# Kernel tuning notes

Hardware: AMD Instinct MI355X
Metric: run time of the kernel (lower is better)

The kernel has to match this reference:

```python
import jax, jax.numpy as jnp
import numpy as np

B, STATE_DIM, MLP_DIM, H, W = 128, 64, 512, 40, 40
LN_EPS = 1e-5


def _sobel_kernel(c):
    # Per-channel depthwise filters in torch order: [c0_sx, c0_sy, c0_id, c1_sx, ...]
    sx = jnp.array([[-1., 0., 1.], [-2., 0., 2.], [-1., 0., 1.]], jnp.float32)
    sy = jnp.array([[-1., -2., -1.], [0., 0., 0.], [1., 2., 1.]], jnp.float32)
    ident = jnp.array([[0., 0., 0.], [0., 1., 0.], [0., 0., 0.]], jnp.float32)
    k = jnp.stack([sx, sy, ident])[:, None]      # [3, 1, 3, 3]
    return jnp.tile(k, (c, 1, 1, 1))             # [3c, 1, 3, 3]


def setup_inputs() -> dict:
    key = jax.random.key(0)
    ks = jax.random.split(key, 6)
    state_in = jax.random.normal(ks[0], (B, STATE_DIM, H, W), jnp.float32)
    w1 = jax.random.normal(ks[1], (MLP_DIM, 3 * STATE_DIM), jnp.float32) * 0.05
    ln_weight = jax.random.uniform(ks[2], (MLP_DIM, H, W), jnp.float32, 0.5, 1.5)
    ln_bias = jax.random.normal(ks[3], (MLP_DIM, H, W), jnp.float32) * 0.01
    w2 = jax.random.normal(ks[4], (STATE_DIM, MLP_DIM), jnp.float32) * 0.05
    mask = jax.random.randint(ks[5], (H, W), 0, 2, jnp.int32)  # bernoulli(0.5) update mask
    return {"state_in": state_in, "w1": w1, "ln_weight": ln_weight,
            "ln_bias": ln_bias, "w2": w2, "mask": mask}


def reference(state_in, w1, ln_weight, ln_bias, w2, mask):
    C = state_in.shape[1]
    # Depthwise 3x3 sobel/identity perception: [B, C, H, W] -> [B, 3C, H, W]
    kern = _sobel_kernel(C)
    x = jax.lax.conv_general_dilated(
        state_in, kern, window_strides=(1, 1), padding='SAME',
        dimension_numbers=('NCHW', 'OIHW', 'NCHW'), feature_group_count=C)
    # 1x1 conv (no bias): [B, 3C, H, W] -> [B, MLP, H, W]
    x = jnp.einsum('bchw,oc->bohw', x, w1)
    # LayerNorm over (MLP, H, W) per sample, with elementwise affine
    mu = jnp.mean(x, axis=(1, 2, 3), keepdims=True)
    var = jnp.var(x, axis=(1, 2, 3), keepdims=True)
    x = (x - mu) * jax.lax.rsqrt(var + LN_EPS) * ln_weight + ln_bias
    x = jax.nn.relu(x)
    # 1x1 conv back to state channels (zero-init in original; random here for testing)
    x = jnp.einsum('bchw,oc->bohw', x, w2)
    # Stochastic per-pixel update mask, broadcast over batch and channels
    x = x * mask.astype(jnp.float32)
    # Alive mask: 3x3 max-pool on alive channel, stride 1, SAME padding
    live = jax.lax.reduce_window(state_in[:, 3], -jnp.inf, jax.lax.max,
                                 (1, 3, 3), (1, 1, 1), 'SAME')
    live = (live > 0.1).astype(jnp.float32)[:, None]  # [B, 1, H, W]
    return state_in + x * live
```

## Files before the change

### kernel.cpp

```cpp
#include <hip/hip_runtime.h>


typedef unsigned short u16;
typedef unsigned int   u32;
typedef __attribute__((ext_vector_type(8))) u16    ushort8;
typedef __attribute__((ext_vector_type(8))) __bf16 bf16x8;
typedef __attribute__((ext_vector_type(4))) float  f32x4;
typedef __attribute__((ext_vector_type(4))) u32    u32x4;

#define NB   128
#define NC   64
#define K1   192
#define NO   512
#define NHW  1600
#define LN_N 819200.0f

__device__ __forceinline__ u16 f2bf(float f) {
    union { float f; u32 u; } v; v.f = f;
    u32 u = v.u;
    u32 r = u + 0x7fffu + ((u >> 16) & 1u);
    return (u16)(r >> 16);
}
__device__ __forceinline__ float bf2f(u16 h) {
    union { u32 u; float f; } v; v.u = ((u32)h) << 16; return v.f;
}
__device__ __forceinline__ f32x4 mfma16(bf16x8 a, bf16x8 b, f32x4 c) {
    return __builtin_amdgcn_mfma_f32_16x16x32_bf16(a, b, c, 0, 0, 0);
}
__device__ __forceinline__ bf16x8 ldfrag(const u16* p) {
    return *(const bf16x8*)p;
}

__device__ __forceinline__ void load_halo(const float* __restrict__ base, int h,
                                          int wq, float reg[3][12]) {
#pragma unroll
    for (int jj = 0; jj < 3; ++jj) {
        int hh = h + jj - 1;
        bool vh = (unsigned)hh < 40u;
        const float* rowp = base + hh * 40;
#pragma unroll
        for (int i = 0; i < 12; ++i) {
            int col = wq * 10 - 1 + i;
            reg[jj][i] = (vh && (unsigned)col < 40u) ? rowp[col] : 0.0f;
        }
    }
}
__device__ __forceinline__ void sobel_px(const float reg[3][12], int t,
                                         float& sx, float& sy, float& idn) {
    sx = (reg[0][t + 2] - reg[0][t]) + 2.0f * (reg[1][t + 2] - reg[1][t])
       + (reg[2][t + 2] - reg[2][t]);
    sy = (reg[2][t] + 2.0f * reg[2][t + 1] + reg[2][t + 2])
       - (reg[0][t] + 2.0f * reg[0][t + 1] + reg[0][t + 2]);
    idn = reg[1][t + 1];
}

__global__ __launch_bounds__(256) void k0_convert(const float* __restrict__ w1,
                                                  const float* __restrict__ w2,
                                                  u16* __restrict__ w1b,
                                                  u16* __restrict__ w2b,
                                                  float* __restrict__ stats) {
    int g = blockIdx.x * 256 + threadIdx.x;
    if (g < NO * K1) {
        w1b[g] = f2bf(w1[g]);
    } else if (g < NO * K1 + NC * NO) {
        w2b[g - NO * K1] = f2bf(w2[g - NO * K1]);
    } else if (g < NO * K1 + NC * NO + 256) {
        stats[g - NO * K1 - NC * NO] = 0.0f;
    }
}

__global__ __launch_bounds__(256) void k0_lncomb(const float* __restrict__ lnw,
                                                 const float* __restrict__ lnb,
                                                 u32* __restrict__ lnc) {
    int g = blockIdx.x * 256 + threadIdx.x;
    u32 w = f2bf(lnw[g]);
    u32 b = f2bf(lnb[g]);
    lnc[g] = (b << 16) | w;
}

__global__ __launch_bounds__(256) void k0_gram(const u16* __restrict__ w1b,
                                               float* __restrict__ G,
                                               float* __restrict__ colw1) {
    int e = blockIdx.x * 256 + threadIdx.x;
    if (e < K1 * K1) {
        int j = e / K1, k = e - j * K1;
        float s = 0.f;
#pragma unroll 8
        for (int o = 0; o < NO; ++o)
            s += bf2f(w1b[o * K1 + j]) * bf2f(w1b[o * K1 + k]);
        G[e] = s;
    } else if (e < K1 * K1 + K1) {
        int k = e - K1 * K1;
        float s = 0.f;
#pragma unroll 8
        for (int o = 0; o < NO; ++o) s += bf2f(w1b[o * K1 + k]);
        colw1[k] = s;
    }
}

__global__ __launch_bounds__(256) void k2_stats(const float* __restrict__ state,
                                                const float* __restrict__ G,
                                                const float* __restrict__ colw1,
                                                float* __restrict__ stats) {
    const int b = blockIdx.x >> 2, quarter = blockIdx.x & 3;
    const int tid = threadIdx.x;
    const int lane = tid & 63, wid = tid >> 6;
    const int q = lane >> 4, l15 = lane & 15;
    const int j0 = (wid & 1) * 96, j1 = (wid >> 1) * 96, jo = wid * 48;

    __shared__ __align__(16) u16 Pt[208 * 104];
    __shared__ float red[8];

    for (int i = tid; i < 208 * 104 / 2; i += 256) ((u32*)Pt)[i] = 0u;
    __syncthreads();
    if (tid < 80) Pt[192 * 104 + tid] = 0x3F80u;

    f32x4 acc[6][6], accO[3];
#pragma unroll
    for (int i = 0; i < 6; ++i)
#pragma unroll
        for (int j = 0; j < 6; ++j) { f32x4 z = {0.f,0.f,0.f,0.f}; acc[i][j] = z; }
#pragma unroll
    for (int j = 0; j < 3; ++j) { f32x4 z = {0.f,0.f,0.f,0.f}; accO[j] = z; }

    const int c = tid >> 2, wq = tid & 3;
    const float* base = state + ((size_t)b * NC + c) * NHW;

    for (int tile = 0; tile < 5; ++tile) {
        const int h0 = (quarter * 5 + tile) * 2;
        __syncthreads();
        for (int rr = 0; rr < 2; ++rr) {
            float reg[3][12];
            load_halo(base, h0 + rr, wq, reg);
#pragma unroll
            for (int t = 0; t < 10; ++t) {
                float sx, sy, idn; sobel_px(reg, t, sx, sy, idn);
                int px = rr * 40 + wq * 10 + t;
                Pt[(3 * c + 0) * 104 + px] = f2bf(sx);
                Pt[(3 * c + 1) * 104 + px] = f2bf(sy);
                Pt[(3 * c + 2) * 104 + px] = f2bf(idn);
            }
        }
        __syncthreads();
#pragma unroll
        for (int ks = 0; ks < 3; ++ks) {
            bf16x8 av[6], bv[6], ao, bo[3];
#pragma unroll
            for (int fi = 0; fi < 6; ++fi)
                av[fi] = ldfrag(&Pt[(j0 + fi * 16 + l15) * 104 + ks * 32 + q * 8]);
#pragma unroll
            for (int fj = 0; fj < 6; ++fj)
                bv[fj] = ldfrag(&Pt[(j1 + fj * 16 + l15) * 104 + ks * 32 + q * 8]);
            ao = ldfrag(&Pt[(192 + l15) * 104 + ks * 32 + q * 8]);
#pragma unroll
            for (int fj = 0; fj < 3; ++fj)
                bo[fj] = ldfrag(&Pt[(jo + fj * 16 + l15) * 104 + ks * 32 + q * 8]);
#pragma unroll
            for (int fi = 0; fi < 6; ++fi)
#pragma unroll
                for (int fj = 0; fj < 6; ++fj)
                    acc[fi][fj] = mfma16(av[fi], bv[fj], acc[fi][fj]);
#pragma unroll
            for (int fj = 0; fj < 3; ++fj)
                accO[fj] = mfma16(ao, bo[fj], accO[fj]);
        }
    }

    float ssq = 0.f;
#pragma unroll
    for (int fi = 0; fi < 6; ++fi)
#pragma unroll
        for (int fj = 0; fj < 6; ++fj) {
            const float* gp = &G[(size_t)(j0 + fi * 16 + q * 4) * K1 + j1 + fj * 16 + l15];
#pragma unroll
            for (int r = 0; r < 4; ++r) ssq += acc[fi][fj][r] * gp[(size_t)r * K1];
        }
    float sm = 0.f;
    if (q == 0) {
#pragma unroll
        for (int fj = 0; fj < 3; ++fj)
            sm += accO[fj][0] * colw1[jo + fj * 16 + l15];
    }
#pragma unroll
    for (int off = 32; off > 0; off >>= 1) {
        ssq += __shfl_down(ssq, off);
        sm  += __shfl_down(sm, off);
    }
    if (lane == 0) { red[wid] = ssq; red[4 + wid] = sm; }
    __syncthreads();
    if (tid == 0) {
        atomicAdd(&stats[b * 2],     red[4] + red[5] + red[6] + red[7]);
        atomicAdd(&stats[b * 2 + 1], red[0] + red[1] + red[2] + red[3]);
    }
}

__global__ void k3_finalize(const float* __restrict__ stats, float2* __restrict__ musig) {
    int t = threadIdx.x;
    if (t < NB) {
        float s = stats[2 * t], qq = stats[2 * t + 1];
        float inv = 1.0f / LN_N;
        float mu = s * inv;
        float var = qq * inv - mu * mu;
        float2 r; r.x = mu; r.y = rsqrtf(var + 1e-5f);
        musig[t] = r;
    }
}

__global__ __launch_bounds__(256, 4) void k4_fused(const float* __restrict__ state,
                                                   const u16* __restrict__ w1b,
                                                   const u16* __restrict__ w2b,
                                                   const u32* __restrict__ lnc,
                                                   const int* __restrict__ mask,
                                                   const float2* __restrict__ musig,
                                                   float* __restrict__ out) {
    const int bx = blockIdx.x;
    const int b  = blockIdx.y;
    const int p0 = bx * 80, h0 = bx * 2;
    const int tid = threadIdx.x;
    const int lane = tid & 63, wid = tid >> 6;
    const int q = lane >> 4, l15 = lane & 15;

    __shared__ __align__(16) u16 Pt[80 * 192];
    __shared__ __align__(16) u16 Ys[80 * 64];
    __shared__ __align__(16) float gate[80];

    const float2 ms = musig[b];
    const float mu = ms.x, rs = ms.y;

    {
        const int c = tid >> 2, wq = tid & 3;
        const float* base = state + ((size_t)b * NC + c) * NHW;
        for (int rr = 0; rr < 2; ++rr) {
            float reg[3][12];
            load_halo(base, h0 + rr, wq, reg);
#pragma unroll
            for (int t = 0; t < 10; ++t) {
                float sx, sy, idn; sobel_px(reg, t, sx, sy, idn);
                int px = rr * 40 + wq * 10 + t;
                int k = 3 * c;
#pragma unroll
                for (int i = 0; i < 3; ++i) {
                    int kk = k + i, u = kk >> 3;
                    int elem = px * 192 + (((u & 0x18) | ((u ^ px) & 7)) << 3) + (kk & 7);
                    Pt[elem] = f2bf(i == 0 ? sx : (i == 1 ? sy : idn));
                }
            }
        }
    }
    if (tid < 80) {
        int p = p0 + tid;
        int h = p / 40, w = p - h * 40;
        const float* st3 = state + ((size_t)b * NC + 3) * NHW;
        float mx = -1e30f;
#pragma unroll
        for (int dh = -1; dh <= 1; ++dh) {
            int hh = h + dh;
            if ((unsigned)hh < 40u)
#pragma unroll
                for (int dw = -1; dw <= 1; ++dw) {
                    int wc = w + dw;
                    if ((unsigned)wc < 40u) mx = fmaxf(mx, st3[hh * 40 + wc]);
                }
        }
        gate[tid] = (mx > 0.1f && mask[p] != 0) ? 1.0f : 0.0f;
    }
    __syncthreads();

    f32x4 acc2[5];
#pragma unroll
    for (int i = 0; i < 5; ++i) { f32x4 z = {0.f,0.f,0.f,0.f}; acc2[i] = z; }

    const int o  = wid * 16 + l15;
    const int sg = wid * 16 + l15;

    for (int oc = 0; oc < 8; ++oc) {
        f32x4 acc1[5];
#pragma unroll
        for (int i = 0; i < 5; ++i) { f32x4 z = {0.f,0.f,0.f,0.f}; acc1[i] = z; }
        const int og = oc * 64 + o;
        bf16x8 bv[6];
#pragma unroll
        for (int ks = 0; ks < 6; ++ks)
            bv[ks] = ldfrag(&w1b[(size_t)og * K1 + ks * 32 + q * 8]);
#pragma unroll
        for (int ks = 0; ks < 6; ++ks) {
#pragma unroll
            for (int mi = 0; mi < 5; ++mi) {
                int r = mi * 16 + l15, u = ks * 4 + q;
                bf16x8 av = ldfrag(&Pt[r * 192 + (((u & 0x18) | ((u ^ r) & 7)) << 3)]);
                acc1[mi] = mfma16(av, bv[ks], acc1[mi]);
            }
        }
#pragma unroll
        for (int mi = 0; mi < 5; ++mi) {
            int pb = mi * 16 + q * 4;
            u32x4 lv = *(const u32x4*)&lnc[(size_t)og * NHW + p0 + pb];
#pragma unroll
            for (int r = 0; r < 4; ++r) {
                float lw = bf2f((u16)(lv[r] & 0xffffu));
                float lb = bf2f((u16)(lv[r] >> 16));
                float y = (acc1[mi][r] - mu) * rs * lw + lb;
                y = fmaxf(y, 0.0f);
                int p = pb + r;
                Ys[p * 64 + ((((o >> 3) ^ p) & 7) << 3) + (o & 7)] = f2bf(y);
            }
        }
        __syncthreads();
        bf16x8 bw[2];
#pragma unroll
        for (int ks2 = 0; ks2 < 2; ++ks2)
            bw[ks2] = ldfrag(&w2b[(size_t)sg * NO + oc * 64 + ks2 * 32 + q * 8]);
#pragma unroll
        for (int ks2 = 0; ks2 < 2; ++ks2) {
#pragma unroll
            for (int mi = 0; mi < 5; ++mi) {
                int r = mi * 16 + l15, u = ks2 * 4 + q;
                bf16x8 av = ldfrag(&Ys[r * 64 + (((u ^ r) & 7) << 3)]);
                acc2[mi] = mfma16(av, bw[ks2], acc2[mi]);
            }
        }
        __syncthreads();
    }

    float* T = (float*)Pt;
#pragma unroll
    for (int mi = 0; mi < 5; ++mi)
#pragma unroll
        for (int r = 0; r < 4; ++r) {
            int p = mi * 16 + q * 4 + r;
            T[sg * 84 + p] = acc2[mi][r];
        }
    __syncthreads();
    {
        int s = tid >> 2, seg = tid & 3;
        size_t obase = ((size_t)b * NC + s) * NHW + p0 + seg * 20;
#pragma unroll
        for (int i = 0; i < 5; ++i) {
            f32x4 st = *(const f32x4*)&state[obase + i * 4];
            f32x4 g  = *(const f32x4*)&gate[seg * 20 + i * 4];
            f32x4 v;
#pragma unroll
            for (int j = 0; j < 4; ++j)
                v[j] = st[j] + g[j] * T[s * 84 + seg * 20 + i * 4 + j];
            *(f32x4*)&out[obase + i * 4] = v;
        }
    }
}

extern "C" void kernel_launch(void* const* d_in, const int* in_sizes, int n_in,
                              void* d_out, int out_size, void* d_ws, size_t ws_size,
                              hipStream_t stream) {
    const float* state = (const float*)d_in[0];
    const float* w1    = (const float*)d_in[1];
    const float* lnw   = (const float*)d_in[2];
    const float* lnb   = (const float*)d_in[3];
    const float* w2    = (const float*)d_in[4];
    const int*   mask  = (const int*)d_in[5];
    float* out = (float*)d_out;

    char* ws = (char*)d_ws;
    u16*    w1b   = (u16*)(ws + 0ull);
    u16*    w2b   = (u16*)(ws + 196608ull);
    u32*    lnc   = (u32*)(ws + 262144ull);
    float*  G     = (float*)(ws + 3538944ull);
    float*  colw1 = (float*)(ws + 3686400ull);
    float*  stats = (float*)(ws + 3687168ull);
    float2* musig = (float2*)(ws + 3688192ull);

    k0_convert <<<513, 256, 0, stream>>>(w1, w2, w1b, w2b, stats);
    k0_lncomb  <<<3200, 256, 0, stream>>>(lnw, lnb, lnc);
    k0_gram    <<<145, 256, 0, stream>>>(w1b, G, colw1);
    k2_stats   <<<512, 256, 0, stream>>>(state, G, colw1, stats);
    k3_finalize<<<1, 128, 0, stream>>>(stats, musig);
    k4_fused   <<<dim3(20, 128), 256, 0, stream>>>(state, w1b, w2b, lnc,
                                                   mask, musig, out);
}
```

Before: 360.8 us.

## Transpose MFMA operands in fused kernel, use MFMA for Gram matrix, write output directly

After: 337.7 us. 1.07x faster.

```diff
diff --git a/kernel.cpp b/kernel.cpp
--- a/kernel.cpp
+++ b/kernel.cpp
@@ -4,6 +4,7 @@
 typedef unsigned short u16;
 typedef unsigned int   u32;
 typedef __attribute__((ext_vector_type(8))) u16    ushort8;
+typedef __attribute__((ext_vector_type(4))) u16    u16x4;
 typedef __attribute__((ext_vector_type(8))) __bf16 bf16x8;
 typedef __attribute__((ext_vector_type(4))) float  f32x4;
 typedef __attribute__((ext_vector_type(4))) u32    u32x4;
@@ -57,11 +58,15 @@
 __global__ __launch_bounds__(256) void k0_convert(const float* __restrict__ w1,
                                                   const float* __restrict__ w2,
                                                   u16* __restrict__ w1b,
+                                                  u16* __restrict__ w1T,
                                                   u16* __restrict__ w2b,
                                                   float* __restrict__ stats) {
     int g = blockIdx.x * 256 + threadIdx.x;
     if (g < NO * K1) {
-        w1b[g] = f2bf(w1[g]);
+        u16 v = f2bf(w1[g]);
+        w1b[g] = v;
+        int o = g / K1, k = g - o * K1;
+        w1T[(size_t)k * NO + o] = v;
     } else if (g < NO * K1 + NC * NO) {
         w2b[g - NO * K1] = f2bf(w2[g - NO * K1]);
     } else if (g < NO * K1 + NC * NO + 256) {
@@ -71,30 +76,49 @@
 
 __global__ __launch_bounds__(256) void k0_lncomb(const float* __restrict__ lnw,
                                                  const float* __restrict__ lnb,
-                                                 u32* __restrict__ lnc) {
-    int g = blockIdx.x * 256 + threadIdx.x;
-    u32 w = f2bf(lnw[g]);
-    u32 b = f2bf(lnb[g]);
-    lnc[g] = (b << 16) | w;
-}
-
-__global__ __launch_bounds__(256) void k0_gram(const u16* __restrict__ w1b,
+                                                 u32* __restrict__ lncT) {
+    __shared__ u32 t[32][33];
+    int p0 = blockIdx.x * 32, o0 = blockIdx.y * 32;
+    int tx = threadIdx.x & 31, ty = threadIdx.x >> 5;
+#pragma unroll
+    for (int k = 0; k < 4; ++k) {
+        size_t gi = (size_t)(o0 + ty + k * 8) * NHW + p0 + tx;
+        t[ty + k * 8][tx] = ((u32)f2bf(lnb[gi]) << 16) | f2bf(lnw[gi]);
+    }
+    __syncthreads();
+#pragma unroll
+    for (int k = 0; k < 4; ++k)
+        lncT[(size_t)(p0 + ty + k * 8) * NO + o0 + tx] = t[tx][ty + k * 8];
+}
+
+__global__ __launch_bounds__(256) void k0_gram(const u16* __restrict__ w1T,
                                                float* __restrict__ G,
                                                float* __restrict__ colw1) {
-    int e = blockIdx.x * 256 + threadIdx.x;
-    if (e < K1 * K1) {
-        int j = e / K1, k = e - j * K1;
+    const int blk = blockIdx.x;
+    const int tid = threadIdx.x;
+    const int lane = tid & 63, wid = tid >> 6;
+    const int q = lane >> 4, l15 = lane & 15;
+    if (blk < 36) {
+        int bj = blk / 6, bk = blk - bj * 6;
+        int j0 = bj * 32 + (wid & 1) * 16, k0 = bk * 32 + (wid >> 1) * 16;
+        f32x4 acc = {0.f, 0.f, 0.f, 0.f};
+#pragma unroll
+        for (int ks = 0; ks < 16; ++ks) {
+            bf16x8 a  = ldfrag(&w1T[(size_t)(j0 + l15) * NO + ks * 32 + q * 8]);
+            bf16x8 bb = ldfrag(&w1T[(size_t)(k0 + l15) * NO + ks * 32 + q * 8]);
+            acc = mfma16(a, bb, acc);
+        }
+#pragma unroll
+        for (int r = 0; r < 4; ++r)
+            G[(size_t)(j0 + q * 4 + r) * K1 + k0 + l15] = acc[r];
+    } else if (tid < K1) {
         float s = 0.f;
-#pragma unroll 8
-        for (int o = 0; o < NO; ++o)
-            s += bf2f(w1b[o * K1 + j]) * bf2f(w1b[o * K1 + k]);
-        G[e] = s;
-    } else if (e < K1 * K1 + K1) {
-        int k = e - K1 * K1;
-        float s = 0.f;
-#pragma unroll 8
-        for (int o = 0; o < NO; ++o) s += bf2f(w1b[o * K1 + k]);
-        colw1[k] = s;
+        for (int i = 0; i < NO / 8; ++i) {
+            ushort8 v = *(const ushort8*)&w1T[(size_t)tid * NO + i * 8];
+#pragma unroll
+            for (int j = 0; j < 8; ++j) s += bf2f(v[j]);
+        }
+        colw1[tid] = s;
     }
 }
 
@@ -171,9 +195,10 @@
     for (int fi = 0; fi < 6; ++fi)
 #pragma unroll
         for (int fj = 0; fj < 6; ++fj) {
-            const float* gp = &G[(size_t)(j0 + fi * 16 + q * 4) * K1 + j1 + fj * 16 + l15];
-#pragma unroll
-            for (int r = 0; r < 4; ++r) ssq += acc[fi][fj][r] * gp[(size_t)r * K1];
+            f32x4 gv = *(const f32x4*)&G[(size_t)(j1 + fj * 16 + l15) * K1
+                                         + j0 + fi * 16 + q * 4];
+#pragma unroll
+            for (int r = 0; r < 4; ++r) ssq += acc[fi][fj][r] * gv[r];
         }
     float sm = 0.f;
     if (q == 0) {
@@ -206,10 +231,10 @@
     }
 }
 
-__global__ __launch_bounds__(256, 4) void k4_fused(const float* __restrict__ state,
+__global__ __launch_bounds__(256, 3) void k4_fused(const float* __restrict__ state,
                                                    const u16* __restrict__ w1b,
                                                    const u16* __restrict__ w2b,
-                                                   const u32* __restrict__ lnc,
+                                                   const u32* __restrict__ lncT,
                                                    const int* __restrict__ mask,
                                                    const float2* __restrict__ musig,
                                                    float* __restrict__ out) {
@@ -221,7 +246,7 @@
     const int q = lane >> 4, l15 = lane & 15;
 
     __shared__ __align__(16) u16 Pt[80 * 192];
-    __shared__ __align__(16) u16 Ys[80 * 64];
+    __shared__ __align__(16) u16 Ys[80 * 128];
     __shared__ __align__(16) float gate[80];
 
     const float2 ms = musig[b];
@@ -266,83 +291,81 @@
     }
     __syncthreads();
 
+    float g5[5];
+#pragma unroll
+    for (int mi = 0; mi < 5; ++mi) g5[mi] = gate[mi * 16 + l15];
+
     f32x4 acc2[5];
 #pragma unroll
     for (int i = 0; i < 5; ++i) { f32x4 z = {0.f,0.f,0.f,0.f}; acc2[i] = z; }
 
-    const int o  = wid * 16 + l15;
-    const int sg = wid * 16 + l15;
-
-    for (int oc = 0; oc < 8; ++oc) {
-        f32x4 acc1[5];
-#pragma unroll
-        for (int i = 0; i < 5; ++i) { f32x4 z = {0.f,0.f,0.f,0.f}; acc1[i] = z; }
-        const int og = oc * 64 + o;
-        bf16x8 bv[6];
-#pragma unroll
-        for (int ks = 0; ks < 6; ++ks)
-            bv[ks] = ldfrag(&w1b[(size_t)og * K1 + ks * 32 + q * 8]);
+    const int ogw = wid * 32;
+
+    for (int oc = 0; oc < 4; ++oc) {
+        const int ob = oc * 128 + ogw;
+        f32x4 acc1[2][5];
+#pragma unroll
+        for (int f = 0; f < 2; ++f)
+#pragma unroll
+            for (int i = 0; i < 5; ++i) { f32x4 z = {0.f,0.f,0.f,0.f}; acc1[f][i] = z; }
 #pragma unroll
         for (int ks = 0; ks < 6; ++ks) {
+            bf16x8 a0 = ldfrag(&w1b[(size_t)(ob + l15) * K1 + ks * 32 + q * 8]);
+            bf16x8 a1 = ldfrag(&w1b[(size_t)(ob + 16 + l15) * K1 + ks * 32 + q * 8]);
 #pragma unroll
             for (int mi = 0; mi < 5; ++mi) {
                 int r = mi * 16 + l15, u = ks * 4 + q;
-                bf16x8 av = ldfrag(&Pt[r * 192 + (((u & 0x18) | ((u ^ r) & 7)) << 3)]);
-                acc1[mi] = mfma16(av, bv[ks], acc1[mi]);
+                bf16x8 bp = ldfrag(&Pt[r * 192 + (((u & 0x18) | ((u ^ r) & 7)) << 3)]);
+                acc1[0][mi] = mfma16(a0, bp, acc1[0][mi]);
+                acc1[1][mi] = mfma16(a1, bp, acc1[1][mi]);
             }
         }
 #pragma unroll
-        for (int mi = 0; mi < 5; ++mi) {
-            int pb = mi * 16 + q * 4;
-            u32x4 lv = *(const u32x4*)&lnc[(size_t)og * NHW + p0 + pb];
-#pragma unroll
-            for (int r = 0; r < 4; ++r) {
-                float lw = bf2f((u16)(lv[r] & 0xffffu));
-                float lb = bf2f((u16)(lv[r] >> 16));
-                float y = (acc1[mi][r] - mu) * rs * lw + lb;
-                y = fmaxf(y, 0.0f);
-                int p = pb + r;
-                Ys[p * 64 + ((((o >> 3) ^ p) & 7) << 3) + (o & 7)] = f2bf(y);
+        for (int f = 0; f < 2; ++f) {
+#pragma unroll
+            for (int mi = 0; mi < 5; ++mi) {
+                int p = mi * 16 + l15;
+                int oglob = ob + f * 16 + q * 4;
+                u32x4 lv = *(const u32x4*)&lncT[(size_t)(p0 + p) * NO + oglob];
+                u16x4 yv;
+#pragma unroll
+                for (int r = 0; r < 4; ++r) {
+                    float lw = bf2f((u16)(lv[r] & 0xffffu));
+                    float lb = bf2f((u16)(lv[r] >> 16));
+                    float y = (acc1[f][mi][r] - mu) * rs * lw + lb;
+                    yv[r] = f2bf(fmaxf(y, 0.0f));
+                }
+                int u = wid * 4 + f * 2 + (q >> 1);
+                int up = u ^ (p & 7);
+                *(u16x4*)&Ys[p * 128 + up * 8 + (q & 1) * 4] = yv;
             }
         }
         __syncthreads();
-        bf16x8 bw[2];
-#pragma unroll
-        for (int ks2 = 0; ks2 < 2; ++ks2)
-            bw[ks2] = ldfrag(&w2b[(size_t)sg * NO + oc * 64 + ks2 * 32 + q * 8]);
-#pragma unroll
-        for (int ks2 = 0; ks2 < 2; ++ks2) {
+#pragma unroll
+        for (int ks2 = 0; ks2 < 4; ++ks2) {
+            bf16x8 aw = ldfrag(&w2b[(size_t)(wid * 16 + l15) * NO
+                                    + oc * 128 + ks2 * 32 + q * 8]);
 #pragma unroll
             for (int mi = 0; mi < 5; ++mi) {
-                int r = mi * 16 + l15, u = ks2 * 4 + q;
-                bf16x8 av = ldfrag(&Ys[r * 64 + (((u ^ r) & 7) << 3)]);
-                acc2[mi] = mfma16(av, bw[ks2], acc2[mi]);
+                int p = mi * 16 + l15;
+                int u = ks2 * 4 + q;
+                int up = u ^ (p & 7);
+                bf16x8 by = ldfrag(&Ys[p * 128 + up * 8]);
+                acc2[mi] = mfma16(aw, by, acc2[mi]);
             }
         }
         __syncthreads();
     }
 
-    float* T = (float*)Pt;
-#pragma unroll
-    for (int mi = 0; mi < 5; ++mi)
+#pragma unroll
+    for (int mi = 0; mi < 5; ++mi) {
+        int p = p0 + mi * 16 + l15;
+        float g = g5[mi];
 #pragma unroll
         for (int r = 0; r < 4; ++r) {
-            int p = mi * 16 + q * 4 + r;
-            T[sg * 84 + p] = acc2[mi][r];
-        }
-    __syncthreads();
-    {
-        int s = tid >> 2, seg = tid & 3;
-        size_t obase = ((size_t)b * NC + s) * NHW + p0 + seg * 20;
-#pragma unroll
-        for (int i = 0; i < 5; ++i) {
-            f32x4 st = *(const f32x4*)&state[obase + i * 4];
-            f32x4 g  = *(const f32x4*)&gate[seg * 20 + i * 4];
-            f32x4 v;
-#pragma unroll
-            for (int j = 0; j < 4; ++j)
-                v[j] = st[j] + g[j] * T[s * 84 + seg * 20 + i * 4 + j];
-            *(f32x4*)&out[obase + i * 4] = v;
+            int s = wid * 16 + q * 4 + r;
+            size_t idx = ((size_t)b * NC + s) * NHW + p;
+            out[idx] = state[idx] + g * acc2[mi][r];
         }
     }
 }
@@ -361,17 +384,18 @@
     char* ws = (char*)d_ws;
     u16*    w1b   = (u16*)(ws + 0ull);
     u16*    w2b   = (u16*)(ws + 196608ull);
-    u32*    lnc   = (u32*)(ws + 262144ull);
-    float*  G     = (float*)(ws + 3538944ull);
-    float*  colw1 = (float*)(ws + 3686400ull);
-    float*  stats = (float*)(ws + 3687168ull);
-    float2* musig = (float2*)(ws + 3688192ull);
-
-    k0_convert <<<513, 256, 0, stream>>>(w1, w2, w1b, w2b, stats);
-    k0_lncomb  <<<3200, 256, 0, stream>>>(lnw, lnb, lnc);
-    k0_gram    <<<145, 256, 0, stream>>>(w1b, G, colw1);
+    u32*    lncT  = (u32*)(ws + 262144ull);
+    u16*    w1T   = (u16*)(ws + 3538944ull);
+    float*  G     = (float*)(ws + 3735552ull);
+    float*  colw1 = (float*)(ws + 3883008ull);
+    float*  stats = (float*)(ws + 3883776ull);
+    float2* musig = (float2*)(ws + 3884800ull);
+
+    k0_convert <<<513, 256, 0, stream>>>(w1, w2, w1b, w1T, w2b, stats);
+    k0_lncomb  <<<dim3(50, 16), 256, 0, stream>>>(lnw, lnb, lncT);
+    k0_gram    <<<37, 256, 0, stream>>>(w1T, G, colw1);
     k2_stats   <<<512, 256, 0, stream>>>(state, G, colw1, stats);
     k3_finalize<<<1, 128, 0, stream>>>(stats, musig);
-    k4_fused   <<<dim3(20, 128), 256, 0, stream>>>(state, w1b, w2b, lnc,
+    k4_fused   <<<dim3(20, 128), 256, 0, stream>>>(state, w1b, w2b, lncT,
                                                    mask, musig, out);
 }
```
